# Optimization experiments

Hardware: AMD Instinct MI355X
Metric: run time of the kernel (lower is better)

## Reference

```python
import jax, jax.numpy as jnp
import numpy as np
import math

B, S, D, H = 4, 2048, 1024, 16
HD = D // H  # head_dim = 64


def setup_inputs() -> dict:
    key = jax.random.key(0)
    ks = jax.random.split(key, 5)
    x = jax.random.normal(ks[0], (B, S, D), dtype=jnp.float32)
    # causal mask, broadcastable over batch and heads
    mask = jnp.tril(jnp.ones((S, S), dtype=bool))[None, None]
    # Linear params in [in, out] layout (math-equivalent to torch's [out, in])
    w_attn = jax.random.normal(ks[1], (D, 3 * D), dtype=jnp.float32) * (1.0 / math.sqrt(D))
    b_attn = jax.random.normal(ks[2], (3 * D,), dtype=jnp.float32) * 0.02
    w_proj = jax.random.normal(ks[3], (D, D), dtype=jnp.float32) * (1.0 / math.sqrt(D))
    b_proj = jax.random.normal(ks[4], (D,), dtype=jnp.float32) * 0.02
    return {"x": x, "mask": mask, "w_attn": w_attn, "b_attn": b_attn,
            "w_proj": w_proj, "b_proj": b_proj}


def reference(x, mask, w_attn, b_attn, w_proj, b_proj):
    b, s, d = x.shape
    # fused qkv projection, then split heads -> [b, h, s, hd]
    qkv = x @ w_attn + b_attn
    q, k, v = jnp.split(qkv, 3, axis=-1)
    split = lambda t: t.reshape(b, s, H, HD).transpose(0, 2, 1, 3)
    q, k, v = split(q), split(k), split(v)
    # scaled dot-product attention with boolean mask (True = keep)
    scores = jnp.einsum('bhqd,bhkd->bhqk', q, k) / math.sqrt(HD)
    scores = jnp.where(mask, scores, -jnp.inf)
    attn = jax.nn.softmax(scores, axis=-1)  # attn_dropout with p=0 is identity
    out = jnp.einsum('bhqk,bhkd->bhqd', attn, v)
    out = out.transpose(0, 2, 1, 3).reshape(b, s, d)
    # output projection (resid_dropout with p=0 is identity)
    return out @ w_proj + b_proj
```

## Files before the change

### kernel.cpp

```cpp
#include <hip/hip_runtime.h>

typedef unsigned short u16;
typedef __attribute__((ext_vector_type(4))) float floatx4;
typedef __attribute__((ext_vector_type(8))) short shortx8;

#define B_ 4
#define S_ 2048
#define D_ 1024
#define H_ 16
#define HD_ 64

__device__ __forceinline__ float b2f(u16 u) {
    return __uint_as_float(((unsigned int)u) << 16);
}
__device__ __forceinline__ u16 f2b(float f) {
    unsigned int u = __float_as_uint(f);
    u += 0x7fffu + ((u >> 16) & 1u);
    return (u16)(u >> 16);
}
__device__ __forceinline__ unsigned long long pack4(float a, float b, float c, float d) {
    return (unsigned long long)f2b(a) | ((unsigned long long)f2b(b) << 16) |
           ((unsigned long long)f2b(c) << 32) | ((unsigned long long)f2b(d) << 48);
}
__device__ __forceinline__ unsigned int permpk(float a, float b) {
    return __builtin_amdgcn_perm(__float_as_uint(b) + 0x8000u,
                                 __float_as_uint(a) + 0x8000u, 0x07060302u);
}
__device__ __forceinline__ void glds16(const u16* g, u16* l) {
    __builtin_amdgcn_global_load_lds(
        (const __attribute__((address_space(1))) unsigned int*)g,
        (__attribute__((address_space(3))) unsigned int*)l, 16, 0, 0);
}

__global__ void detect_dtype(const unsigned int* __restrict__ x, int* __restrict__ flag) {
    const int l = threadIdx.x;
    int cnt = 0;
    for (int i = l; i < 4096; i += 64) {
        const unsigned int e = (x[i] >> 7) & 0xffu;
        cnt += (e >= 110u && e <= 134u) ? 1 : 0;
    }
#pragma unroll
    for (int d = 1; d < 64; d <<= 1) cnt += __shfl_xor(cnt, d);
    if (l == 0) *flag = (cnt > 2048) ? 1 : 0;
}

__global__ __launch_bounds__(256) void convert_x(const void* __restrict__ xin,
                                                 u16* __restrict__ xb,
                                                 const void* __restrict__ bA,
                                                 const void* __restrict__ bP,
                                                 u16* __restrict__ bAb,
                                                 u16* __restrict__ bPb,
                                                 const int* __restrict__ flag) {
    const int isbf = *flag;
    const size_t i = ((size_t)blockIdx.x * 256 + threadIdx.x) * 8;
    if (isbf) {
        *(uint4*)(xb + i) = *(const uint4*)((const u16*)xin + i);
    } else {
        const float* xf = (const float*)xin;
        float4 a = *(const float4*)(xf + i);
        float4 b = *(const float4*)(xf + i + 4);
        u16 o[8] = {f2b(a.x), f2b(a.y), f2b(a.z), f2b(a.w),
                    f2b(b.x), f2b(b.y), f2b(b.z), f2b(b.w)};
        *(uint4*)(xb + i) = *(uint4*)o;
    }
    if (blockIdx.x == 0) {
        for (int j = threadIdx.x; j < 3072; j += 256)
            bAb[j] = isbf ? ((const u16*)bA)[j] : f2b(((const float*)bA)[j]);
        for (int j = threadIdx.x; j < 1024; j += 256)
            bPb[j] = isbf ? ((const u16*)bP)[j] : f2b(((const float*)bP)[j]);
    }
}

__global__ __launch_bounds__(256) void transpose_both(const void* __restrict__ inA,
                                                      u16* __restrict__ outA,
                                                      const void* __restrict__ inP,
                                                      u16* __restrict__ outP,
                                                      const int* __restrict__ flag) {
    const int isbf = *flag;
    __shared__ u16 tile[32][33];
    const int tx = threadIdx.x & 31;
    const int ty = threadIdx.x >> 5;
    int bxi = blockIdx.x;
    const void* in;
    u16* out;
    int N;
    if (bxi < 96) { in = inA; out = outA; N = 3072; }
    else          { in = inP; out = outP; N = 1024; bxi -= 96; }
    const int K = 1024;
    const int bx = bxi * 32;
    const int by = blockIdx.y * 32;
    if (isbf) {
#pragma unroll
        for (int i = 0; i < 32; i += 8)
            tile[ty + i][tx] = ((const u16*)in)[(size_t)(by + ty + i) * N + bx + tx];
    } else {
#pragma unroll
        for (int i = 0; i < 32; i += 8)
            tile[ty + i][tx] = f2b(((const float*)in)[(size_t)(by + ty + i) * N + bx + tx]);
    }
    __syncthreads();
#pragma unroll
    for (int i = 0; i < 32; i += 8)
        out[(size_t)(bx + ty + i) * K + by + tx] = tile[tx][ty + i];
}

template <int MODE>
__global__ __launch_bounds__(256) void gemm_bt(const u16* __restrict__ A,
                                               const u16* __restrict__ BT,
                                               const u16* __restrict__ bias,
                                               void* __restrict__ outv,
                                               int M, int N, int K,
                                               u16* __restrict__ qws,
                                               u16* __restrict__ kws,
                                               u16* __restrict__ vws,
                                               const int* __restrict__ flag) {
    __shared__ __align__(16) u16 As[2][128 * 32];
    __shared__ __align__(16) u16 Bs[2][128 * 32];

    const int isbf = (MODE == 0) ? *flag : 1;
    const int tid = threadIdx.x;
    const int w = tid >> 6, l = tid & 63;
    const int lane_m = l & 15, quad = l >> 4;
    const int bm = blockIdx.x * 128, bn = blockIdx.y * 128;
    const int wm = (w >> 1) * 64, wn = (w & 1) * 64;

    floatx4 acc[4][4];
#pragma unroll
    for (int i = 0; i < 4; i++)
#pragma unroll
        for (int j = 0; j < 4; j++) acc[i][j] = (floatx4){0.f, 0.f, 0.f, 0.f};

    const int lr = l >> 2, sl = l & 3;
    const int cA = sl ^ ((lr >> 1) & 3);
    const int rb0 = w * 16, rb1 = 64 + w * 16;
    const u16* Arow0 = A + (size_t)(bm + rb0 + lr) * K + cA * 8;
    const u16* Arow1 = A + (size_t)(bm + rb1 + lr) * K + cA * 8;
    const u16* Brow0 = BT + (size_t)(bn + rb0 + lr) * K + cA * 8;
    const u16* Brow1 = BT + (size_t)(bn + rb1 + lr) * K + cA * 8;

    auto stage = [&](int t) {
        const int k0 = t * 32;
        u16* ad = &As[t & 1][0];
        u16* bd = &Bs[t & 1][0];
        glds16(Arow0 + k0, ad + rb0 * 32);
        glds16(Arow1 + k0, ad + rb1 * 32);
        glds16(Brow0 + k0, bd + rb0 * 32);
        glds16(Brow1 + k0, bd + rb1 * 32);
    };

    const int NT = K >> 5;
    stage(0);
    for (int t = 0; t < NT; ++t) {
        __syncthreads();
        if (t + 1 < NT) stage(t + 1);

        const u16* Ac = &As[t & 1][0];
        const u16* Bc = &Bs[t & 1][0];
        shortx8 af[4], bf[4];
#pragma unroll
        for (int mb = 0; mb < 4; mb++) {
            const int r = wm + mb * 16 + lane_m;
            af[mb] = *(const shortx8*)(Ac + r * 32 + (quad ^ ((r >> 1) & 3)) * 8);
        }
#pragma unroll
        for (int nb = 0; nb < 4; nb++) {
            const int r = wn + nb * 16 + lane_m;
            bf[nb] = *(const shortx8*)(Bc + r * 32 + (quad ^ ((r >> 1) & 3)) * 8);
        }
#pragma unroll
        for (int mb = 0; mb < 4; mb++)
#pragma unroll
            for (int nb = 0; nb < 4; nb++)
                acc[mb][nb] = __builtin_amdgcn_mfma_f32_16x16x32_bf16(
                    af[mb], bf[nb], acc[mb][nb], 0, 0, 0);
    }

    const float SCALE_Q = 0.18033688011112042f;

    if (MODE == 1 && (bn >> 10) == 2) {
        __syncthreads();
        u16* ep = (w < 2) ? &As[w][0] : &Bs[w - 2][0];
#pragma unroll
        for (int nb = 0; nb < 4; nb++) {
            const int lhd = nb * 16 + lane_m;
            const float bv = b2f(bias[bn + wn + lhd]);
            const int sw = (lhd & 7) << 3;
#pragma unroll
            for (int mb = 0; mb < 4; mb++) {
                const int o = mb * 16 + quad * 4;
                unsigned long long pk =
                    pack4(acc[mb][nb][0] + bv, acc[mb][nb][1] + bv,
                          acc[mb][nb][2] + bv, acc[mb][nb][3] + bv);
                *(unsigned long long*)(ep + lhd * 64 + (o ^ sw)) = pk;
            }
        }
        __syncthreads();
        const int bI = bm >> 11;
        const int hI = ((bn + wn) >> 6) & 15;
        const int s0 = (bm & 2047) + wm;
        u16* vb0 = vws + (size_t)(bI * 16 + hI) * 64 * 2048;
        const int rr8 = l >> 3, c8 = l & 7;
#pragma unroll
        for (int p = 0; p < 8; p++) {
            const int lhd = p * 8 + rr8;
            uint4 v4 = *(const uint4*)(ep + lhd * 64 + ((c8 << 3) ^ ((lhd & 7) << 3)));
            *(uint4*)(vb0 + (size_t)lhd * 2048 + s0 + c8 * 8) = v4;
        }
    } else {
#pragma unroll
        for (int nb = 0; nb < 4; nb++) {
            const int col = bn + wn + nb * 16 + lane_m;
            const float bv = b2f(bias[col]);
#pragma unroll
            for (int mb = 0; mb < 4; mb++) {
                const int rowb = bm + wm + mb * 16 + quad * 4;
#pragma unroll
                for (int r = 0; r < 4; r++) {
                    float v = acc[mb][nb][r] + bv;
                    const int rr = rowb + r;
                    if (MODE == 0) {
                        if (isbf) ((u16*)outv)[(size_t)rr * N + col] = f2b(v);
                        else ((float*)outv)[(size_t)rr * N + col] = v;
                    } else {
                        const int which = col >> 10;
                        if (which == 0) v *= SCALE_Q;
                        const int h = (col >> 6) & 15;
                        const int hd = col & 63;
                        const int b = rr >> 11, s = rr & 2047;
                        u16* dst = which == 0 ? qws : kws;
                        dst[((size_t)(b * 16 + h) * 2048 + s) * 64 + hd] = f2b(v);
                    }
                }
            }
        }
    }
}

__global__ __launch_bounds__(512, 4) void attn_kernel(const u16* __restrict__ Qg,
                                                      const u16* __restrict__ Kg,
                                                      const u16* __restrict__ Vtg,
                                                      u16* __restrict__ Og) {
    __shared__ __align__(16) u16 Ks[2][64 * 64];
    __shared__ __align__(16) u16 Vs[2][64 * 64];
    __shared__ __align__(16) u16 Ps[8][16 * 72];

    const int tid = threadIdx.x, w = tid >> 6, l = tid & 63;
    const int lane_m = l & 15, quad = l >> 4;
    const int bh = blockIdx.y;
    const u16* qp = Qg + (size_t)bh * S_ * 64;
    const u16* kp = Kg + (size_t)bh * S_ * 64;
    const u16* vtp = Vtg + (size_t)bh * 64 * S_;
    u16* psw = &Ps[w][0];
    const int b = bh >> 4, h = bh & 15;

    const int lr8 = l >> 3, sl8 = l & 7;
    const int cK = sl8 ^ (lr8 & 7);
    const int rbase = w * 8;
    const u16* Kr = kp + (size_t)(rbase + lr8) * 64 + cK * 8;
    const u16* Vr = vtp + (size_t)(rbase + lr8) * S_ + cK * 8;

    auto stage = [&](int t) {
        const int k0 = t * 64;
        glds16(Kr + (size_t)k0 * 64, &Ks[t & 1][0] + rbase * 64);
        glds16(Vr + k0, &Vs[t & 1][0] + rbase * 64);
    };

    for (int pass = 0; pass < 2; pass++) {
        const int xm = pass ? (15 - (int)blockIdx.x) : (int)blockIdx.x;
        const int q0 = xm * 128;
        const int qw0 = q0 + w * 16;

        shortx8 qF[2];
#pragma unroll
        for (int ks = 0; ks < 2; ks++)
            qF[ks] = *(const shortx8*)(qp + (size_t)(qw0 + lane_m) * 64 + ks * 32 + quad * 8);

        floatx4 o_acc[4];
#pragma unroll
        for (int md = 0; md < 4; md++) o_acc[md] = (floatx4){0.f, 0.f, 0.f, 0.f};
        float m_i = -1e30f, l_i = 0.f;

        const int ntiles = (q0 >> 6) + 2;
        const int myend = qw0 + 15;

        __syncthreads();
        stage(0);
        for (int t = 0; t < ntiles; t++) {
            const int k0 = t * 64;
            __syncthreads();
            if (t + 1 < ntiles) stage(t + 1);

            if (k0 <= myend) {
                const u16* kb = &Ks[t & 1][0];
                const u16* vb = &Vs[t & 1][0];
                floatx4 sc[4];
#pragma unroll
                for (int mb = 0; mb < 4; mb++) sc[mb] = (floatx4){0.f, 0.f, 0.f, 0.f};
#pragma unroll
                for (int ks = 0; ks < 2; ks++) {
                    shortx8 kA[4];
#pragma unroll
                    for (int mb = 0; mb < 4; mb++) {
                        const int r = mb * 16 + lane_m;
                        kA[mb] = *(const shortx8*)(kb + r * 64 + (((ks * 4 + quad) ^ (r & 7)) * 8));
                    }
                    __builtin_amdgcn_s_setprio(1);
#pragma unroll
                    for (int mb = 0; mb < 4; mb++)
                        sc[mb] = __builtin_amdgcn_mfma_f32_16x16x32_bf16(
                            kA[mb], qF[ks], sc[mb], 0, 0, 0);
                    __builtin_amdgcn_s_setprio(0);
                }

                const int qg = qw0 + lane_m;
                if (k0 + 63 > qw0) {
#pragma unroll
                    for (int mb = 0; mb < 4; mb++)
#pragma unroll
                        for (int r = 0; r < 4; r++) {
                            const int kvg = k0 + mb * 16 + quad * 4 + r;
                            if (kvg > qg) sc[mb][r] = -1e30f;
                        }
                }
                float mloc = -1e30f;
#pragma unroll
                for (int mb = 0; mb < 4; mb++) {
                    float a = fmaxf(fmaxf(sc[mb][0], sc[mb][1]),
                                    fmaxf(sc[mb][2], sc[mb][3]));
                    mloc = fmaxf(mloc, a);
                }
                mloc = fmaxf(mloc, __shfl_xor(mloc, 16));
                mloc = fmaxf(mloc, __shfl_xor(mloc, 32));
                float mnew = m_i;
                if (!__all(mloc <= m_i + 8.0f)) {
                    mnew = fmaxf(m_i, mloc);
                    const float alpha = __builtin_amdgcn_exp2f(m_i - mnew);
                    m_i = mnew;
                    l_i *= alpha;
#pragma unroll
                    for (int md = 0; md < 4; md++) o_acc[md] *= alpha;
                }
                float psum = 0.f;
#pragma unroll
                for (int mb = 0; mb < 4; mb++) {
                    const float p0 = __builtin_amdgcn_exp2f(sc[mb][0] - mnew);
                    const float p1 = __builtin_amdgcn_exp2f(sc[mb][1] - mnew);
                    const float p2 = __builtin_amdgcn_exp2f(sc[mb][2] - mnew);
                    const float p3 = __builtin_amdgcn_exp2f(sc[mb][3] - mnew);
                    psum += (p0 + p1) + (p2 + p3);
                    uint2 pk = {permpk(p0, p1), permpk(p2, p3)};
                    *(uint2*)(psw + lane_m * 72 + mb * 16 + quad * 4) = pk;
                }
                psum += __shfl_xor(psum, 16);
                psum += __shfl_xor(psum, 32);
                l_i += psum;

#pragma unroll
                for (int ks = 0; ks < 2; ks++) {
                    shortx8 vF[4], pF;
#pragma unroll
                    for (int md = 0; md < 4; md++) {
                        const int r = md * 16 + lane_m;
                        vF[md] = *(const shortx8*)(vb + r * 64 + (((ks * 4 + quad) ^ (r & 7)) * 8));
                    }
                    pF = *(const shortx8*)(psw + lane_m * 72 + ks * 32 + quad * 8);
                    __builtin_amdgcn_s_setprio(1);
#pragma unroll
                    for (int md = 0; md < 4; md++)
                        o_acc[md] = __builtin_amdgcn_mfma_f32_16x16x32_bf16(
                            vF[md], pF, o_acc[md], 0, 0, 0);
                    __builtin_amdgcn_s_setprio(0);
                }
            }
        }

        {
            const float inv = 1.0f / l_i;
            const int qg = qw0 + lane_m;
            const size_t base = ((size_t)b * 2048 + qg) * 1024 + h * 64;
#pragma unroll
            for (int md = 0; md < 4; md++) {
                *(unsigned long long*)(Og + base + md * 16 + quad * 4) =
                    pack4(o_acc[md][0] * inv, o_acc[md][1] * inv,
                          o_acc[md][2] * inv, o_acc[md][3] * inv);
            }
        }
    }
}

extern "C" void kernel_launch(void* const* d_in, const int* in_sizes, int n_in,
                              void* d_out, int out_size, void* d_ws, size_t ws_size,
                              hipStream_t stream) {
    const void* x      = d_in[0];
    const void* w_attn = d_in[2];
    const void* b_attn = d_in[3];
    const void* w_proj = d_in[4];
    const void* b_proj = d_in[5];

    u16* qws = (u16*)d_ws;
    u16* kws = qws + 8388608;
    u16* vws = kws + 8388608;
    u16* xb  = vws + 8388608;
    u16* aws = xb;
    u16* wtA = xb + 8388608;
    u16* wtP = wtA + 3145728;
    u16* bAb = wtP + 1048576;
    u16* bPb = bAb + 3072;
    int* flag = (int*)(bPb + 1024);

    detect_dtype<<<1, 64, 0, stream>>>((const unsigned int*)x, flag);
    convert_x<<<4096, 256, 0, stream>>>(x, xb, b_attn, b_proj, bAb, bPb, flag);
    transpose_both<<<dim3(128, 32), 256, 0, stream>>>(w_attn, wtA, w_proj, wtP, flag);

    gemm_bt<1><<<dim3(8192 / 128, 3072 / 128), 256, 0, stream>>>(
        xb, wtA, bAb, nullptr, 8192, 3072, 1024, qws, kws, vws, flag);

    attn_kernel<<<dim3(8, B_ * H_), 512, 0, stream>>>(qws, kws, vws, aws);

    gemm_bt<0><<<dim3(8192 / 128, 1024 / 128), 256, 0, stream>>>(
        aws, wtP, bPb, d_out, 8192, 1024, 1024, nullptr, nullptr, nullptr, flag);
}
```

Baseline: 292.9 us.

## Triple-buffer LDS staging with explicit vmcnt waits in GEMM and attention

Switches the GEMM and attention kernels from double to triple-buffered LDS tiles, issuing loads two tiles ahead. The full __syncthreads is replaced by partial s_waitcnt vmcnt waits plus a raw s_barrier, so the next tile's global-to-LDS loads can stay in flight during compute. This aims to hide global memory latency. It costs extra LDS, which may lower occupancy, especially for the attention kernel declared with launch bounds of 4 blocks. It also depends on the vmcnt counts exactly matching the number of outstanding loads per thread.

```diff
diff --git a/kernel.cpp b/kernel.cpp
--- a/kernel.cpp
+++ b/kernel.cpp
@@ -31,6 +31,14 @@
         (const __attribute__((address_space(1))) unsigned int*)g,
         (__attribute__((address_space(3))) unsigned int*)l, 16, 0, 0);
 }
+__device__ __forceinline__ void bar() {
+    asm volatile("" ::: "memory");
+    __builtin_amdgcn_s_barrier();
+    asm volatile("" ::: "memory");
+}
+#define VMW4 asm volatile("s_waitcnt vmcnt(4)" ::: "memory")
+#define VMW2 asm volatile("s_waitcnt vmcnt(2)" ::: "memory")
+#define VMW0 asm volatile("s_waitcnt vmcnt(0)" ::: "memory")
 
 __global__ void detect_dtype(const unsigned int* __restrict__ x, int* __restrict__ flag) {
     const int l = threadIdx.x;
@@ -114,8 +122,8 @@
                                                u16* __restrict__ kws,
                                                u16* __restrict__ vws,
                                                const int* __restrict__ flag) {
-    __shared__ __align__(16) u16 As[2][128 * 32];
-    __shared__ __align__(16) u16 Bs[2][128 * 32];
+    __shared__ __align__(16) u16 As[3][128 * 32];
+    __shared__ __align__(16) u16 Bs[3][128 * 32];
 
     const int isbf = (MODE == 0) ? *flag : 1;
     const int tid = threadIdx.x;
@@ -140,8 +148,8 @@
 
     auto stage = [&](int t) {
         const int k0 = t * 32;
-        u16* ad = &As[t & 1][0];
-        u16* bd = &Bs[t & 1][0];
+        u16* ad = &As[t % 3][0];
+        u16* bd = &Bs[t % 3][0];
         glds16(Arow0 + k0, ad + rb0 * 32);
         glds16(Arow1 + k0, ad + rb1 * 32);
         glds16(Brow0 + k0, bd + rb0 * 32);
@@ -150,12 +158,14 @@
 
     const int NT = K >> 5;
     stage(0);
+    stage(1);
     for (int t = 0; t < NT; ++t) {
-        __syncthreads();
-        if (t + 1 < NT) stage(t + 1);
-
-        const u16* Ac = &As[t & 1][0];
-        const u16* Bc = &Bs[t & 1][0];
+        if (t < NT - 1) { VMW4; } else { VMW0; }
+        bar();
+        if (t + 2 < NT) stage(t + 2);
+
+        const u16* Ac = &As[t % 3][0];
+        const u16* Bc = &Bs[t % 3][0];
         shortx8 af[4], bf[4];
 #pragma unroll
         for (int mb = 0; mb < 4; mb++) {
@@ -240,8 +250,8 @@
                                                       const u16* __restrict__ Kg,
                                                       const u16* __restrict__ Vtg,
                                                       u16* __restrict__ Og) {
-    __shared__ __align__(16) u16 Ks[2][64 * 64];
-    __shared__ __align__(16) u16 Vs[2][64 * 64];
+    __shared__ __align__(16) u16 Ks[3][64 * 64];
+    __shared__ __align__(16) u16 Vs[3][64 * 64];
     __shared__ __align__(16) u16 Ps[8][16 * 72];
 
     const int tid = threadIdx.x, w = tid >> 6, l = tid & 63;
@@ -261,8 +271,8 @@
 
     auto stage = [&](int t) {
         const int k0 = t * 64;
-        glds16(Kr + (size_t)k0 * 64, &Ks[t & 1][0] + rbase * 64);
-        glds16(Vr + k0, &Vs[t & 1][0] + rbase * 64);
+        glds16(Kr + (size_t)k0 * 64, &Ks[t % 3][0] + rbase * 64);
+        glds16(Vr + k0, &Vs[t % 3][0] + rbase * 64);
     };
 
     for (int pass = 0; pass < 2; pass++) {
@@ -285,14 +295,16 @@
 
         __syncthreads();
         stage(0);
+        stage(1);
         for (int t = 0; t < ntiles; t++) {
             const int k0 = t * 64;
-            __syncthreads();
-            if (t + 1 < ntiles) stage(t + 1);
+            if (t < ntiles - 1) { VMW2; } else { VMW0; }
+            bar();
+            if (t + 2 < ntiles) stage(t + 2);
 
             if (k0 <= myend) {
-                const u16* kb = &Ks[t & 1][0];
-                const u16* vb = &Vs[t & 1][0];
+                const u16* kb = &Ks[t % 3][0];
+                const u16* vb = &Vs[t % 3][0];
                 floatx4 sc[4];
 #pragma unroll
                 for (int mb = 0; mb < 4; mb++) sc[mb] = (floatx4){0.f, 0.f, 0.f, 0.f};
```

New measurement: 296.6 us. About the same (+1.2%).
